# Optimization experiments

Measured on AMD Instinct MI355X. Metric: run time of the kernel, lower is better.

The kernel has to match this reference:

```python
import jax, jax.numpy as jnp
import numpy as np

NUM_LEVELS = 2
THETA = 0.5
EPS = 1e-5  # torch F.instance_norm default eps


def _patch_sigmoid_attn(x, p):
    # Non-overlapping patch instance-norm + sigmoid. For p==0 (n=1) this is a
    # full per-(B,C) instance norm, matching the original p==0 branch.
    B, C, H, W = x.shape
    n = 2 ** p                      # patches per spatial dim (kh==sh => fold is a reshape)
    sph, spw = H // n, W // n       # patch size
    xp = x.reshape(B, C, n, sph, n, spw)
    mu = xp.mean(axis=(3, 5), keepdims=True)
    var = xp.var(axis=(3, 5), keepdims=True)  # biased var, as in torch instance_norm
    w = jax.nn.sigmoid((xp - mu) * jax.lax.rsqrt(var + EPS))
    return w.reshape(B, C, H, W)


def setup_inputs() -> dict:
    key = jax.random.key(0)
    k1, _ = jax.random.split(key)
    x = jax.random.normal(k1, (8, 64, 256, 256), dtype=jnp.float32)
    level_weights = jnp.ones((NUM_LEVELS + 1,), dtype=jnp.float32) / (NUM_LEVELS + 1)
    return {"x": x, "level_weights": level_weights}


def reference(x, level_weights):
    feats = []
    for p in range(NUM_LEVELS, -1, -1):  # coarse-to-fine, p=0 last (order matters for weights)
        w = _patch_sigmoid_attn(x, p)
        feats.append(THETA * x + (1.0 - THETA) * w * x)
    lw = jax.nn.softmax(level_weights)
    out = lw[0] * feats[0]
    for i in range(1, NUM_LEVELS + 1):
        out = out + lw[i] * feats[i]
    return out
```

## Files before the change

kernel.cpp:

```cpp
#include <hip/hip_runtime.h>

#define EPS 1e-5f

__global__ __launch_bounds__(256) void k_patch_stats(const float4* __restrict__ x4,
                                                     float2* __restrict__ part) {
    const int P    = blockIdx.x;
    const int bc   = P >> 4;
    const int pidx = P & 15;
    const int pr   = pidx >> 2, pc = pidx & 3;
    const int t    = threadIdx.x;
    const long chan4 = (long)bc << 14;

    float s = 0.f, ss = 0.f;
#pragma unroll
    for (int k = 0; k < 4; ++k) {
        const int q    = k * 256 + t;
        const int row  = q >> 4;
        const int col4 = q & 15;
        const long idx = chan4 + (long)(pr * 64 + row) * 64 + pc * 16 + col4;
        const float4 v = x4[idx];
        s  += v.x + v.y + v.z + v.w;
        ss += v.x * v.x + v.y * v.y + v.z * v.z + v.w * v.w;
    }
#pragma unroll
    for (int off = 32; off > 0; off >>= 1) {
        s  += __shfl_down(s, off, 64);
        ss += __shfl_down(ss, off, 64);
    }
    __shared__ float2 red[4];
    const int wave = t >> 6, lane = t & 63;
    if (lane == 0) red[wave] = make_float2(s, ss);
    __syncthreads();
    if (t == 0) {
        float S = 0.f, SS = 0.f;
#pragma unroll
        for (int i = 0; i < 4; ++i) { S += red[i].x; SS += red[i].y; }
        part[P] = make_float2(S, SS);
    }
}

__global__ __launch_bounds__(64) void k_aggregate(const float2* __restrict__ part,
                                                  float2* __restrict__ S) {
    const int bc = blockIdx.x;
    const int t  = threadIdx.x;
    __shared__ float2 ps[16];
    if (t < 16) ps[t] = part[bc * 16 + t];
    __syncthreads();

    float sum = 0.f, sq = 0.f, n = 1.f;
    int slot = -1;
    if (t < 16) {
        sum = ps[t].x; sq = ps[t].y; n = 4096.f; slot = t;
    } else if (t < 20) {
        const int g = t - 16, gr = g >> 1, gc = g & 1;
        const int b = 8 * gr + 2 * gc;
        sum = ps[b].x + ps[b + 1].x + ps[b + 4].x + ps[b + 5].x;
        sq  = ps[b].y + ps[b + 1].y + ps[b + 4].y + ps[b + 5].y;
        n = 16384.f; slot = 16 + g;
    } else if (t == 20) {
#pragma unroll
        for (int i = 0; i < 16; ++i) { sum += ps[i].x; sq += ps[i].y; }
        n = 65536.f; slot = 20;
    }
    if (slot >= 0) {
        const float mu   = sum / n;
        const float var  = sq / n - mu * mu;
        const float rstd = rsqrtf(var + EPS);
        S[bc * 21 + slot] = make_float2(rstd, -mu * rstd);
    }
}

__device__ __forceinline__ float sigm(float t) {
    return __builtin_amdgcn_rcpf(1.f + __expf(-t));
}

__global__ __launch_bounds__(256) void k_out(const float4* __restrict__ x4,
                                             const float2* __restrict__ S,
                                             const float* __restrict__ lw,
                                             float4* __restrict__ out4) {
    const long i = (long)blockIdx.x * 256 + threadIdx.x;

    const float w0 = lw[0], w1 = lw[1], w2 = lw[2];
    const float m  = fmaxf(w0, fmaxf(w1, w2));
    const float e0 = __expf(w0 - m), e1 = __expf(w1 - m), e2 = __expf(w2 - m);
    const float inv = __builtin_amdgcn_rcpf(e0 + e1 + e2);
    const float lwA = e0 * inv;
    const float lwB = e1 * inv;
    const float lwC = e2 * inv;

    const int bc = (int)(i >> 14);
    const int f  = (int)(i & 16383);
    const int w4 = f & 63;
    const int h  = f >> 6;
    const float2* Sc = S + bc * 21;
    const float2 s2 = Sc[(h >> 6) * 4 + (w4 >> 4)];
    const float2 s1 = Sc[16 + (h >> 7) * 2 + (w4 >> 5)];
    const float2 s0 = Sc[20];

    const float4 v = x4[i];
    float4 r;
#define ELT(comp)                                                              \
    {                                                                          \
        const float xv  = v.comp;                                              \
        const float acc = lwA * sigm(fmaf(xv, s2.x, s2.y))                     \
                        + lwB * sigm(fmaf(xv, s1.x, s1.y))                     \
                        + lwC * sigm(fmaf(xv, s0.x, s0.y));                    \
        r.comp = xv * (0.5f + 0.5f * acc);                                     \
    }
    ELT(x) ELT(y) ELT(z) ELT(w)
#undef ELT
    out4[i] = r;
}

extern "C" void kernel_launch(void* const* d_in, const int* in_sizes, int n_in,
                              void* d_out, int out_size, void* d_ws, size_t ws_size,
                              hipStream_t stream) {
    const float* x  = (const float*)d_in[0];
    const float* lw = (const float*)d_in[1];
    float* out      = (float*)d_out;

    float2* part = (float2*)d_ws;
    float2* S    = part + 8192;

    k_patch_stats<<<8192, 256, 0, stream>>>((const float4*)x, part);
    k_aggregate<<<512, 64, 0, stream>>>(part, S);
    k_out<<<32768, 256, 0, stream>>>((const float4*)x, S, lw, (float4*)out);
}
```

Measured before the change: 249.5 us.

## Fuse patch stats, aggregation and output into one per-channel kernel

Replaces the three-kernel pipeline (patch statistics, aggregation, elementwise output) with a single kernel where each block owns one (B,C) channel. The block computes all 16 patch sums, derives the 21 normalization coefficients in shared memory, then rereads its channel to write the output, hoping the reread hits cache. The three sigmoids are also merged algebraically into one reciprocal using exp2 with LOG2E folded into the coefficients. The trade-off is only 512 blocks with little occupancy to hide memory latency, and a serialized stats-then-output phase inside each block.

```diff
diff --git a/kernel.cpp b/kernel.cpp
--- a/kernel.cpp
+++ b/kernel.cpp
@@ -1,115 +1,115 @@
 #include <hip/hip_runtime.h>
 
 #define EPS 1e-5f
+#define LOG2E 1.4426950408889634f
 
-__global__ __launch_bounds__(256) void k_patch_stats(const float4* __restrict__ x4,
-                                                     float2* __restrict__ part) {
-    const int P    = blockIdx.x;
-    const int bc   = P >> 4;
-    const int pidx = P & 15;
-    const int pr   = pidx >> 2, pc = pidx & 3;
+__global__ __launch_bounds__(256) void k_fused(const float4* __restrict__ x4,
+                                               const float* __restrict__ lw,
+                                               float4* __restrict__ out4) {
+    const int bc   = blockIdx.x;
     const int t    = threadIdx.x;
-    const long chan4 = (long)bc << 14;
+    const int wave = t >> 6;
+    const int lane = t & 63;
+    const int pc   = lane >> 4;
+    const long base = (long)bc << 14;
 
-    float s = 0.f, ss = 0.f;
+    __shared__ float2 red[4][16];
+    __shared__ float2 psum[16];
+    __shared__ float2 coef[21];
+
+    float2 acc[4];
 #pragma unroll
-    for (int k = 0; k < 4; ++k) {
-        const int q    = k * 256 + t;
-        const int row  = q >> 4;
-        const int col4 = q & 15;
-        const long idx = chan4 + (long)(pr * 64 + row) * 64 + pc * 16 + col4;
-        const float4 v = x4[idx];
-        s  += v.x + v.y + v.z + v.w;
-        ss += v.x * v.x + v.y * v.y + v.z * v.z + v.w * v.w;
+    for (int pr = 0; pr < 4; ++pr) {
+        float s = 0.f, q = 0.f;
+#pragma unroll
+        for (int kk = 0; kk < 16; ++kk) {
+            const float4 v = x4[base + (pr * 16 + kk) * 256 + t];
+            s += v.x + v.y + v.z + v.w;
+            q += v.x * v.x + v.y * v.y + v.z * v.z + v.w * v.w;
+        }
+        acc[pr] = make_float2(s, q);
     }
 #pragma unroll
-    for (int off = 32; off > 0; off >>= 1) {
-        s  += __shfl_down(s, off, 64);
-        ss += __shfl_down(ss, off, 64);
+    for (int off = 1; off < 16; off <<= 1) {
+#pragma unroll
+        for (int pr = 0; pr < 4; ++pr) {
+            acc[pr].x += __shfl_xor(acc[pr].x, off, 64);
+            acc[pr].y += __shfl_xor(acc[pr].y, off, 64);
+        }
     }
-    __shared__ float2 red[4];
-    const int wave = t >> 6, lane = t & 63;
-    if (lane == 0) red[wave] = make_float2(s, ss);
+    if ((lane & 15) == 0) {
+#pragma unroll
+        for (int pr = 0; pr < 4; ++pr) red[wave][pr * 4 + pc] = acc[pr];
+    }
     __syncthreads();
-    if (t == 0) {
-        float S = 0.f, SS = 0.f;
+    if (t < 16) {
+        float2 s = red[0][t];
 #pragma unroll
-        for (int i = 0; i < 4; ++i) { S += red[i].x; SS += red[i].y; }
-        part[P] = make_float2(S, SS);
+        for (int w = 1; w < 4; ++w) { s.x += red[w][t].x; s.y += red[w][t].y; }
+        psum[t] = s;
     }
-}
-
-__global__ __launch_bounds__(64) void k_aggregate(const float2* __restrict__ part,
-                                                  float2* __restrict__ S) {
-    const int bc = blockIdx.x;
-    const int t  = threadIdx.x;
-    __shared__ float2 ps[16];
-    if (t < 16) ps[t] = part[bc * 16 + t];
     __syncthreads();
-
-    float sum = 0.f, sq = 0.f, n = 1.f;
-    int slot = -1;
-    if (t < 16) {
-        sum = ps[t].x; sq = ps[t].y; n = 4096.f; slot = t;
-    } else if (t < 20) {
-        const int g = t - 16, gr = g >> 1, gc = g & 1;
-        const int b = 8 * gr + 2 * gc;
-        sum = ps[b].x + ps[b + 1].x + ps[b + 4].x + ps[b + 5].x;
-        sq  = ps[b].y + ps[b + 1].y + ps[b + 4].y + ps[b + 5].y;
-        n = 16384.f; slot = 16 + g;
-    } else if (t == 20) {
+    if (t < 21) {
+        float sum, sq, n;
+        if (t < 16) {
+            sum = psum[t].x; sq = psum[t].y; n = 4096.f;
+        } else if (t < 20) {
+            const int g = t - 16, gr = g >> 1, gc = g & 1;
+            const int b = 8 * gr + 2 * gc;
+            sum = psum[b].x + psum[b + 1].x + psum[b + 4].x + psum[b + 5].x;
+            sq  = psum[b].y + psum[b + 1].y + psum[b + 4].y + psum[b + 5].y;
+            n = 16384.f;
+        } else {
+            sum = 0.f; sq = 0.f;
 #pragma unroll
-        for (int i = 0; i < 16; ++i) { sum += ps[i].x; sq += ps[i].y; }
-        n = 65536.f; slot = 20;
-    }
-    if (slot >= 0) {
+            for (int i = 0; i < 16; ++i) { sum += psum[i].x; sq += psum[i].y; }
+            n = 65536.f;
+        }
         const float mu   = sum / n;
         const float var  = sq / n - mu * mu;
         const float rstd = rsqrtf(var + EPS);
-        S[bc * 21 + slot] = make_float2(rstd, -mu * rstd);
+        coef[t] = make_float2(-rstd * LOG2E, mu * rstd * LOG2E);
     }
-}
-
-__device__ __forceinline__ float sigm(float t) {
-    return __builtin_amdgcn_rcpf(1.f + __expf(-t));
-}
-
-__global__ __launch_bounds__(256) void k_out(const float4* __restrict__ x4,
-                                             const float2* __restrict__ S,
-                                             const float* __restrict__ lw,
-                                             float4* __restrict__ out4) {
-    const long i = (long)blockIdx.x * 256 + threadIdx.x;
 
     const float w0 = lw[0], w1 = lw[1], w2 = lw[2];
-    const float m  = fmaxf(w0, fmaxf(w1, w2));
-    const float e0 = __expf(w0 - m), e1 = __expf(w1 - m), e2 = __expf(w2 - m);
-    const float inv = __builtin_amdgcn_rcpf(e0 + e1 + e2);
-    const float lwA = e0 * inv;
-    const float lwB = e1 * inv;
-    const float lwC = e2 * inv;
+    const float mx  = fmaxf(w0, fmaxf(w1, w2));
+    const float ex0 = __expf(w0 - mx), ex1 = __expf(w1 - mx), ex2 = __expf(w2 - mx);
+    const float inv = __builtin_amdgcn_rcpf(ex0 + ex1 + ex2);
+    const float lwA = ex0 * inv;
+    const float lwB = ex1 * inv;
+    const float lwC = ex2 * inv;
 
-    const int bc = (int)(i >> 14);
-    const int f  = (int)(i & 16383);
-    const int w4 = f & 63;
-    const int h  = f >> 6;
-    const float2* Sc = S + bc * 21;
-    const float2 s2 = Sc[(h >> 6) * 4 + (w4 >> 4)];
-    const float2 s1 = Sc[16 + (h >> 7) * 2 + (w4 >> 5)];
-    const float2 s0 = Sc[20];
+    __syncthreads();
 
-    const float4 v = x4[i];
-    float4 r;
+#pragma unroll
+    for (int kb = 0; kb < 4; ++kb) {
+        const float2 c2 = coef[kb * 4 + pc];
+        const float2 c1 = coef[16 + (kb >> 1) * 2 + (pc >> 1)];
+        const float2 c0 = coef[20];
+#pragma unroll 4
+        for (int kk = 0; kk < 16; ++kk) {
+            const long idx = base + (kb * 16 + kk) * 256 + t;
+            const float4 v = x4[idx];
+            float4 r;
 #define ELT(comp)                                                              \
-    {                                                                          \
-        const float xv  = v.comp;                                              \
-        const float acc = lwA * sigm(fmaf(xv, s2.x, s2.y))                     \
-                        + lwB * sigm(fmaf(xv, s1.x, s1.y))                     \
-                        + lwC * sigm(fmaf(xv, s0.x, s0.y));                    \
-        r.comp = xv * (0.5f + 0.5f * acc);                                     \
+            {                                                                  \
+                const float xv = v.comp;                                       \
+                const float e2 = __builtin_amdgcn_exp2f(fmaf(xv, c2.x, c2.y)); \
+                const float e1 = __builtin_amdgcn_exp2f(fmaf(xv, c1.x, c1.y)); \
+                const float e0 = __builtin_amdgcn_exp2f(fmaf(xv, c0.x, c0.y)); \
+                const float pA = 1.f + e2, pB = 1.f + e1, pC = 1.f + e0;       \
+                const float mBC = pB * pC, mAB = pA * pB;                      \
+                const float mAC = pA * pC;                                     \
+                const float num = fmaf(lwA, mBC, fmaf(lwB, mAC, lwC * mAB));   \
+                const float den = mAB * pC;                                    \
+                const float t0  = 0.5f * xv;                                   \
+                r.comp = fmaf(t0 * num, __builtin_amdgcn_rcpf(den), t0);       \
+            }
+            ELT(x) ELT(y) ELT(z) ELT(w)
+#undef ELT
+            out4[idx] = r;
+        }
     }
-    ELT(x) ELT(y) ELT(z) ELT(w)
-#undef ELT
-    out4[i] = r;
 }
 
 extern "C" void kernel_launch(void* const* d_in, const int* in_sizes, int n_in,
@@ -118,11 +118,5 @@
     const float* x  = (const float*)d_in[0];
     const float* lw = (const float*)d_in[1];
     float* out      = (float*)d_out;
-
-    float2* part = (float2*)d_ws;
-    float2* S    = part + 8192;
-
-    k_patch_stats<<<8192, 256, 0, stream>>>((const float4*)x, part);
-    k_aggregate<<<512, 64, 0, stream>>>(part, S);
-    k_out<<<32768, 256, 0, stream>>>((const float4*)x, S, lw, (float4*)out);
+    k_fused<<<512, 256, 0, stream>>>((const float4*)x, lw, (float4*)out);
 }
```

New measurement: 249.8 us. Within noise of the previous version (+0.1%).
